# Performance work log

Hardware: AMD Instinct MI355X
Metric: run time of the kernel (lower is better)

## Reference

```python
import jax, jax.numpy as jnp
import numpy as np

H = 512      # hidden_size (hardcoded in prior split)
L = 3        # num_layers
NH = 8       # num_heads
B = 16384    # batch
LN_EPS = 1e-5


def layer_norm(x, g, b):
    m = x.mean(-1, keepdims=True)
    v = ((x - m) ** 2).mean(-1, keepdims=True)
    return (x - m) / jnp.sqrt(v + LN_EPS) * g + b


def cross_gen(src, tgt, ipw, ipb, qkv_w, qkv_b, ao_w, ao_b,
              ln1g, ln1b, ln2g, ln2b, f1w, f1b, f2w, f2b, opw, opb, rw):
    """CrossModalGenerator.forward(src, tgt) for the whole batch (seq_len == 1)."""
    bsz = src.shape[0]
    dh = H // NH
    x = src @ ipw.T + ipb  # input_proj
    for l in range(L):
        wq, wk, wv = jnp.split(qkv_w[l], 3, axis=0)
        bq, bk, bv = jnp.split(qkv_b[l], 3)
        q = (x @ wq.T + bq).reshape(bsz, NH, dh)
        k = (tgt @ wk.T + bk).reshape(bsz, NH, dh)
        v = (tgt @ wv.T + bv).reshape(bsz, NH, dh)
        # single key/value token -> softmax over 1 element == 1 (kept for faithful grads)
        scores = (q * k).sum(-1, keepdims=True) / jnp.sqrt(jnp.float32(dh))  # [B,NH,1]
        w = jax.nn.softmax(scores, axis=-1)
        attn = (w * v).reshape(bsz, H)
        attn = attn @ ao_w[l].T + ao_b[l]  # MHA out_proj
        x = layer_norm(x + attn, ln1g[l], ln1b[l])
        h = jax.nn.gelu(x @ f1w[l].T + f1b[l], approximate=False)
        h = h @ f2w[l].T + f2b[l]
        x = layer_norm(x + h, ln2g[l], ln2b[l])
    gen = x @ opw.T + opb  # output_proj
    return rw * tgt + (1.0 - rw) * gen


def setup_inputs() -> dict:
    key = jax.random.key(0)
    ks = iter(jax.random.split(key, 40))
    nk = lambda: next(ks)
    s = jnp.float32(0.02)  # weight scale for numerical sanity
    f32 = jnp.float32
    return {
        "image_features": jax.random.normal(nk(), (B, H), f32),
        "text_features": jax.random.normal(nk(), (B, H), f32),
        "g_ipw": jax.random.normal(nk(), (2, H, H), f32) * s,
        "g_ipb": jnp.zeros((2, H), f32),
        "g_qkv_w": jax.random.normal(nk(), (2, L, 3 * H, H), f32) * s,
        "g_qkv_b": jnp.zeros((2, L, 3 * H), f32),
        "g_ao_w": jax.random.normal(nk(), (2, L, H, H), f32) * s,
        "g_ao_b": jnp.zeros((2, L, H), f32),
        "g_ln1g": jnp.ones((2, L, H), f32),
        "g_ln1b": jnp.zeros((2, L, H), f32),
        "g_ln2g": jnp.ones((2, L, H), f32),
        "g_ln2b": jnp.zeros((2, L, H), f32),
        "g_f1w": jax.random.normal(nk(), (2, L, 4 * H, H), f32) * s,
        "g_f1b": jnp.zeros((2, L, 4 * H), f32),
        "g_f2w": jax.random.normal(nk(), (2, L, H, 4 * H), f32) * s,
        "g_f2b": jnp.zeros((2, L, H), f32),
        "g_opw": jax.random.normal(nk(), (2, H, H), f32) * s,
        "g_opb": jnp.zeros((2, H), f32),
        "g_rw": jnp.full((2,), 0.5, f32),  # residual_weight per generator
        "prior_w1": jax.random.normal(nk(), (2 * H, H), f32) * s,
        "prior_b1": jnp.zeros((2 * H,), f32),
        "prior_w2": jax.random.normal(nk(), (2 * H, 2 * H), f32) * s,
        "prior_b2": jnp.zeros((2 * H,), f32),
        "prior_emb": jax.random.normal(nk(), (1, H), f32),
        "missing_type": jax.random.randint(nk(), (B,), 0, 4, jnp.int32),
    }


def reference(image_features, text_features, g_ipw, g_ipb, g_qkv_w, g_qkv_b,
              g_ao_w, g_ao_b, g_ln1g, g_ln1b, g_ln2g, g_ln2b, g_f1w, g_f1b,
              g_f2w, g_f2b, g_opw, g_opb, g_rw, prior_w1, prior_b1, prior_w2,
              prior_b2, prior_emb, missing_type):
    def gen(i, src, tgt):
        return cross_gen(src, tgt, g_ipw[i], g_ipb[i], g_qkv_w[i], g_qkv_b[i],
                         g_ao_w[i], g_ao_b[i], g_ln1g[i], g_ln1b[i],
                         g_ln2g[i], g_ln2b[i], g_f1w[i], g_f1b[i],
                         g_f2w[i], g_f2b[i], g_opw[i], g_opb[i], g_rw[i])

    # MoE-style dense dispatch: run both generators on the full batch, select by type.
    gen_text = gen(0, image_features, text_features)  # img_to_text, missing_type==1
    gen_img = gen(1, text_features, image_features)   # text_to_img, missing_type==2

    prior = jax.nn.gelu(prior_emb @ prior_w1.T + prior_b1, approximate=False)
    prior = prior @ prior_w2.T + prior_b2  # [1, 2H]
    p_img, p_text = prior[:, :H], prior[:, H:]

    mt = missing_type[:, None]
    enhanced_img = jnp.where(mt == 2, gen_img, image_features)
    enhanced_img = jnp.where(mt == 3, p_img, enhanced_img)
    enhanced_text = jnp.where(mt == 1, gen_text, text_features)
    enhanced_text = jnp.where(mt == 3, p_text, enhanced_text)
    return enhanced_img, enhanced_text
```

## Files before the change

### kernel.cpp

```cpp
#include <hip/hip_runtime.h>
#include <hip/hip_bf16.h>
#include <math.h>

#define BDIM 16384
#define HDIM 512

typedef __bf16 bf16;
typedef float f32x4 __attribute__((ext_vector_type(4)));
typedef __bf16 bf16x8 __attribute__((ext_vector_type(8)));
typedef __bf16 bf16x4 __attribute__((ext_vector_type(4)));


__device__ __forceinline__ void gload16(const bf16* g, bf16* l) {
  __builtin_amdgcn_global_load_lds((const __attribute__((address_space(1))) void*)g,
                                   (__attribute__((address_space(3))) void*)l, 16, 0, 0);
}

__device__ __forceinline__ float gelu_exact(float x) {
  return 0.5f * x * (1.0f + erff(x * 0.70710678118654752f));
}
__device__ __forceinline__ float gelu_fast(float x) {
  float u = x * (0.7978845608f + 0.0356774081f * x * x);
  float e = __expf(2.f * u);
  float t = 1.f - 2.f / (e + 1.f);
  return 0.5f * x * (1.f + t);
}


__global__ void cvt_f32_bf16(const float* __restrict__ src, bf16* __restrict__ dst, int n4) {
  int i = blockIdx.x * blockDim.x + threadIdx.x;
  if (i >= n4) return;
  f32x4 v = *(const f32x4*)(src + (size_t)i * 4);
  bf16x4 o;
  o[0] = (bf16)v[0]; o[1] = (bf16)v[1]; o[2] = (bf16)v[2]; o[3] = (bf16)v[3];
  *(bf16x4*)(dst + (size_t)i * 4) = o;
}

__global__ void cvt_wvT(const float* __restrict__ qkv, bf16* __restrict__ dst) {
  __shared__ float t[32][33];
  int il = blockIdx.z;
  int bm = blockIdx.x * 32;
  int bk = blockIdx.y * 32;
  const float* s = qkv + (size_t)il * 786432 + 524288;
  int tx = threadIdx.x & 31, ty = threadIdx.x >> 5;
#pragma unroll
  for (int j = 0; j < 4; ++j)
    t[ty * 4 + j][tx] = s[(size_t)(bm + ty * 4 + j) * 512 + bk + tx];
  __syncthreads();
  bf16* d = dst + (size_t)il * 262144;
#pragma unroll
  for (int j = 0; j < 4; ++j)
    d[(size_t)(bk + ty * 4 + j) * 512 + bm + tx] = (bf16)t[tx][ty * 4 + j];
}

__global__ void zfill(float* __restrict__ p, int n) {
  int i = blockIdx.x * 256 + threadIdx.x;
  if (i < n) p[i] = 0.f;
}

__global__ void bias_combine(const float* __restrict__ aow, const float* __restrict__ qkvb,
                             const float* __restrict__ aob, float* __restrict__ bc) {
  int gid = blockIdx.x * 4 + (threadIdx.x >> 6);
  int il = gid >> 9;
  int lane = threadIdx.x & 63;
  const float* ar = aow + (size_t)gid * 512 + lane * 8;
  const float* bv = qkvb + il * 1536 + 1024 + lane * 8;
  float s = 0.f;
#pragma unroll
  for (int i = 0; i < 8; ++i) s += ar[i] * bv[i];
#pragma unroll
  for (int off = 32; off > 0; off >>= 1) s += __shfl_xor(s, off);
  if (lane == 0) bc[gid] = s + aob[gid];
}


template<int ACT, bool RES, int K>
__launch_bounds__(256, 2)
__global__ void gemm_q(const bf16* __restrict__ A, long long Az,
                       const bf16* __restrict__ W, long long Wz,
                       const float* __restrict__ bias, long long bz,
                       const bf16* X, long long Xz,
                       bf16* C, long long Cz, int ldc) {
  __shared__ bf16 lds[3][12288];
  const long long z = blockIdx.z;
  A += z * Az; W += z * Wz; bias += z * bz; C += z * Cz;
  if (RES) X += z * Xz;
  const int tid = threadIdx.x, lane = tid & 63, wid = tid >> 6;
  const int brow = blockIdx.x * 128, bcol = blockIdx.y * 256;
  const int wn = wid * 64, lr = lane & 15, kg = lane >> 4;
  const int ko = (kg ^ ((lr >> 1) & 3)) << 3;

  f32x4 acc[8][4] = {};

  const int sco = (((tid & 3) ^ ((tid >> 3) & 3)) << 3);
  const bf16* Ag = A + (size_t)(brow + (tid >> 2)) * K + sco;
  const bf16* Wg = W + (size_t)(bcol + (tid >> 2)) * K + sco;
  auto SA = [&](int s, int kt, int u) {
    gload16(Ag + (size_t)u * 64 * K + kt * 32, &lds[s][u * 2048 + wid * 512]);
  };
  auto SB = [&](int s, int kt, int u) {
    gload16(Wg + (size_t)u * 64 * K + kt * 32, &lds[s][4096 + u * 2048 + wid * 512]);
  };

  const int nt = K / 32;
  SA(0,0,0); SA(0,0,1); SB(0,0,0); SB(0,0,1); SB(0,0,2); SB(0,0,3);
  SA(1,1,0); SA(1,1,1); SB(1,1,0); SB(1,1,1); SB(1,1,2); SB(1,1,3);

  int slot = 0;
  for (int t = 0; t < nt; ++t) {
    int s2 = slot + 2; if (s2 >= 3) s2 -= 3;
    const bf16* LA = &lds[slot][0];
    const bf16* LB = &lds[slot][4096];
    if (t + 2 < nt) { SA(s2,t+2,0); SA(s2,t+2,1); SB(s2,t+2,0); SB(s2,t+2,1); }
    if (t + 2 < nt)      asm volatile("s_waitcnt vmcnt(10)" ::: "memory");
    else if (t + 1 < nt) asm volatile("s_waitcnt vmcnt(6)" ::: "memory");
    else                 asm volatile("s_waitcnt vmcnt(0)" ::: "memory");
    __builtin_amdgcn_s_barrier();
    bf16x8 a[8], b0, b1;
#pragma unroll
    for (int m = 0; m < 8; ++m) a[m] = *(const bf16x8*)(LA + ((m*16+lr)<<5) + ko);
    b0 = *(const bf16x8*)(LB + ((wn + lr)<<5) + ko);
    b1 = *(const bf16x8*)(LB + ((wn + 16 + lr)<<5) + ko);
    __builtin_amdgcn_s_setprio(1);
#pragma unroll
    for (int m = 0; m < 8; ++m) {
      acc[m][0] = __builtin_amdgcn_mfma_f32_16x16x32_bf16(b0, a[m], acc[m][0], 0, 0, 0);
      acc[m][1] = __builtin_amdgcn_mfma_f32_16x16x32_bf16(b1, a[m], acc[m][1], 0, 0, 0);
    }
    __builtin_amdgcn_s_setprio(0);
    asm volatile("" ::: "memory");
    __builtin_amdgcn_s_barrier();
    if (t + 2 < nt) { SB(s2,t+2,2); SB(s2,t+2,3); }
    bf16x8 b2 = *(const bf16x8*)(LB + ((wn + 32 + lr)<<5) + ko);
    bf16x8 b3 = *(const bf16x8*)(LB + ((wn + 48 + lr)<<5) + ko);
    __builtin_amdgcn_s_setprio(1);
#pragma unroll
    for (int m = 0; m < 8; ++m) {
      acc[m][2] = __builtin_amdgcn_mfma_f32_16x16x32_bf16(b2, a[m], acc[m][2], 0, 0, 0);
      acc[m][3] = __builtin_amdgcn_mfma_f32_16x16x32_bf16(b3, a[m], acc[m][3], 0, 0, 0);
    }
    __builtin_amdgcn_s_setprio(0);
    asm volatile("" ::: "memory");
    __builtin_amdgcn_s_barrier();
    slot += 1; if (slot >= 3) slot = 0;
  }

  f32x4 bv4[4];
#pragma unroll
  for (int n = 0; n < 4; ++n)
    bv4[n] = *(const f32x4*)(bias + bcol + wn + n * 16 + kg * 4);
#pragma unroll
  for (int m = 0; m < 8; ++m) {
    int row = brow + m * 16 + lr;
#pragma unroll
    for (int n = 0; n < 4; ++n) {
      int col = bcol + wn + n * 16 + kg * 4;
      f32x4 v;
#pragma unroll
      for (int j = 0; j < 4; ++j) {
        float t = acc[m][n][j] + bv4[n][j];
        if (ACT == 1) t = gelu_fast(t);
        v[j] = t;
      }
      if (RES) {
        bf16x4 xv = *(const bf16x4*)(X + (size_t)row * 512 + col);
#pragma unroll
        for (int j = 0; j < 4; ++j) v[j] += (float)xv[j];
      }
      bf16x4 o;
#pragma unroll
      for (int j = 0; j < 4; ++j) o[j] = (bf16)v[j];
      *(bf16x4*)(C + (size_t)row * ldc + col) = o;
    }
  }
}


__launch_bounds__(256)
__global__ void gemm128(const bf16* __restrict__ A, long long Az, int lda,
                        const bf16* __restrict__ W, long long Wz,
                        const float* __restrict__ bias, long long bz,
                        bf16* __restrict__ C, long long Cz, int ldc, int K) {
  __shared__ bf16 As[128 * 64];
  __shared__ bf16 Bs[128 * 64];
  const long long z = blockIdx.z;
  A += z * Az; W += z * Wz; bias += z * bz; C += z * Cz;
  const int tid = threadIdx.x;
  const int lane = tid & 63;
  const int wid = tid >> 6;
  const int brow = blockIdx.x * 128;
  const int bcol = blockIdx.y * 128;
  const int wr = (wid >> 1) * 64;
  const int wc = (wid & 1) * 64;
  const int lr = lane & 15;
  const int kg = lane >> 4;
  f32x4 acc[4][4] = {};
  const bf16* Abase = A + (size_t)(brow + (tid >> 3)) * lda + ((tid & 7) << 3);
  const bf16* Wbase = W + (size_t)(bcol + (tid >> 3)) * K + ((tid & 7) << 3);
  bf16* AsDst = As + wid * 512;
  bf16* BsDst = Bs + wid * 512;
  for (int k0 = 0; k0 < K; k0 += 64) {
#pragma unroll
    for (int j = 0; j < 4; ++j) {
      gload16(Abase + (size_t)j * 32 * lda + k0, AsDst + j * 2048);
      gload16(Wbase + (size_t)j * 32 * K + k0, BsDst + j * 2048);
    }
    __syncthreads();
#pragma unroll
    for (int kk = 0; kk < 64; kk += 32) {
      bf16x8 a[4], bq[4];
#pragma unroll
      for (int m = 0; m < 4; ++m)
        a[m] = *(const bf16x8*)(As + (wr + m * 16 + lr) * 64 + kk + kg * 8);
#pragma unroll
      for (int n = 0; n < 4; ++n)
        bq[n] = *(const bf16x8*)(Bs + (wc + n * 16 + lr) * 64 + kk + kg * 8);
#pragma unroll
      for (int m = 0; m < 4; ++m)
#pragma unroll
        for (int n = 0; n < 4; ++n)
          acc[m][n] = __builtin_amdgcn_mfma_f32_16x16x32_bf16(a[m], bq[n], acc[m][n], 0, 0, 0);
    }
    __syncthreads();
  }
  float bv[4];
#pragma unroll
  for (int n = 0; n < 4; ++n) bv[n] = bias[bcol + wc + n * 16 + lr];
#pragma unroll
  for (int m = 0; m < 4; ++m) {
    int row = brow + wr + m * 16 + kg * 4;
#pragma unroll
    for (int n = 0; n < 4; ++n) {
      int col = bcol + wc + n * 16 + lr;
#pragma unroll
      for (int j = 0; j < 4; ++j)
        C[(size_t)(row + j) * ldc + col] = (bf16)(acc[m][n][j] + bv[n]);
    }
  }
}


template<int MODE>
__global__ void ln_chain(const bf16* __restrict__ Y, const bf16* __restrict__ R,
                         const float* __restrict__ gA, const float* __restrict__ bA,
                         const float* __restrict__ gB, const float* __restrict__ bB,
                         bf16* __restrict__ O) {
  int lane = threadIdx.x & 63;
  int row = blockIdx.x * 4 + (threadIdx.x >> 6);
  int gen = row >> 14;
  size_t base = (size_t)row * HDIM + lane * 8;
  bf16x8 yv = *(const bf16x8*)(Y + base);
  float v[8], s = 0.f, q = 0.f;
#pragma unroll
  for (int i = 0; i < 8; ++i) { v[i] = (float)yv[i]; s += v[i]; q += v[i] * v[i]; }
#pragma unroll
  for (int off = 32; off > 0; off >>= 1) { s += __shfl_xor(s, off); q += __shfl_xor(q, off); }
  float mean = s * (1.f / HDIM);
  float rstd = rsqrtf(q * (1.f / HDIM) - mean * mean + 1e-5f);
  const float* gAp = gA + gen * 1536 + lane * 8;
  const float* bAp = bA + gen * 1536 + lane * 8;
  if (MODE == 0) {
    bf16x8 o;
#pragma unroll
    for (int i = 0; i < 8; ++i) o[i] = (bf16)((v[i] - mean) * rstd * gAp[i] + bAp[i]);
    *(bf16x8*)(O + base) = o;
    return;
  }
  bf16x8 rv = *(const bf16x8*)(R + base);
  float u[8]; s = 0.f; q = 0.f;
#pragma unroll
  for (int i = 0; i < 8; ++i) {
    u[i] = (v[i] - mean) * rstd * gAp[i] + bAp[i] + (float)rv[i];
    s += u[i]; q += u[i] * u[i];
  }
#pragma unroll
  for (int off = 32; off > 0; off >>= 1) { s += __shfl_xor(s, off); q += __shfl_xor(q, off); }
  float m2 = s * (1.f / HDIM);
  float r2 = rsqrtf(q * (1.f / HDIM) - m2 * m2 + 1e-5f);
  const float* gBp = gB + gen * 1536 + lane * 8;
  const float* bBp = bB + gen * 1536 + lane * 8;
  bf16x8 o;
#pragma unroll
  for (int i = 0; i < 8; ++i) o[i] = (bf16)((u[i] - m2) * r2 * gBp[i] + bBp[i]);
  *(bf16x8*)(O + base) = o;
}


__global__ void prior_fc1(const float* __restrict__ emb, const float* __restrict__ w1,
                          const float* __restrict__ b1, float* __restrict__ h) {
  int j = blockIdx.x * 4 + (threadIdx.x >> 6);
  int lane = threadIdx.x & 63;
  const float* wr = w1 + (size_t)j * 512 + lane * 8;
  const float* e = emb + lane * 8;
  float s = 0.f;
#pragma unroll
  for (int i = 0; i < 8; ++i) s += e[i] * wr[i];
#pragma unroll
  for (int off = 32; off > 0; off >>= 1) s += __shfl_xor(s, off);
  if (lane == 0) h[j] = gelu_exact(s + b1[j]);
}

__global__ void prior_fc2(const float* __restrict__ h, const float* __restrict__ w2,
                          const float* __restrict__ b2, float* __restrict__ p) {
  int j = blockIdx.x * 4 + (threadIdx.x >> 6);
  int lane = threadIdx.x & 63;
  const float* wr = w2 + (size_t)j * 1024 + lane * 16;
  const float* e = h + lane * 16;
  float s = 0.f;
#pragma unroll
  for (int i = 0; i < 16; ++i) s += e[i] * wr[i];
#pragma unroll
  for (int off = 32; off > 0; off >>= 1) s += __shfl_xor(s, off);
  if (lane == 0) p[j] = s + b2[j];
}


__global__ void combine(const float* __restrict__ img, const float* __restrict__ txt,
                        const bf16* __restrict__ gen_t, const bf16* __restrict__ gen_i,
                        const float* __restrict__ prior, const int* __restrict__ mt,
                        const float* __restrict__ rw, float* __restrict__ out) {
  int i4 = blockIdx.x * blockDim.x + threadIdx.x;
  if (i4 >= BDIM * 128) return;
  int bb = i4 >> 7;
  int c = (i4 & 127) << 2;
  size_t idx = (size_t)bb * HDIM + c;
  int m = mt[bb];
  f32x4 iv = *(const f32x4*)(img + idx);
  f32x4 tv = *(const f32x4*)(txt + idx);
  f32x4 oi = iv, ot = tv;
  if (m == 2) {
    float r = rw[1];
    bf16x4 gv = *(const bf16x4*)(gen_i + idx);
#pragma unroll
    for (int k = 0; k < 4; ++k) oi[k] = r * iv[k] + (1.f - r) * (float)gv[k];
  } else if (m == 3) {
    oi = *(const f32x4*)(prior + c);
  }
  if (m == 1) {
    float r = rw[0];
    bf16x4 gv = *(const bf16x4*)(gen_t + idx);
#pragma unroll
    for (int k = 0; k < 4; ++k) ot[k] = r * tv[k] + (1.f - r) * (float)gv[k];
  } else if (m == 3) {
    ot = *(const f32x4*)(prior + 512 + c);
  }
  *(f32x4*)(out + idx) = oi;
  *(f32x4*)(out + (size_t)BDIM * HDIM + idx) = ot;
}


extern "C" void kernel_launch(void* const* d_in, const int* in_sizes, int n_in,
                              void* d_out, int out_size, void* d_ws, size_t ws_size,
                              hipStream_t stream) {
  const float* img  = (const float*)d_in[0];
  const float* txt  = (const float*)d_in[1];
  const float* ipw  = (const float*)d_in[2];
  const float* ipb  = (const float*)d_in[3];
  const float* qkvw = (const float*)d_in[4];
  const float* qkvb = (const float*)d_in[5];
  const float* aow  = (const float*)d_in[6];
  const float* aob  = (const float*)d_in[7];
  const float* ln1g = (const float*)d_in[8];
  const float* ln1b = (const float*)d_in[9];
  const float* ln2g = (const float*)d_in[10];
  const float* ln2b = (const float*)d_in[11];
  const float* f1w  = (const float*)d_in[12];
  const float* f1b  = (const float*)d_in[13];
  const float* f2w  = (const float*)d_in[14];
  const float* f2b  = (const float*)d_in[15];
  const float* opw  = (const float*)d_in[16];
  const float* opb  = (const float*)d_in[17];
  const float* rw   = (const float*)d_in[18];
  const float* pw1  = (const float*)d_in[19];
  const float* pb1  = (const float*)d_in[20];
  const float* pw2  = (const float*)d_in[21];
  const float* pb2  = (const float*)d_in[22];
  const float* pemb = (const float*)d_in[23];
  const int*   mt   = (const int*)d_in[24];
  float* out = (float*)d_out;

  const size_t B = BDIM;
  char* ws = (char*)d_ws;
  size_t off = 0;
  auto alloc = [&](size_t bytes) -> char* {
    char* p = ws + off;
    off += (bytes + 255) & ~(size_t)255;
    return p;
  };
  bf16* src_bf = (bf16*)alloc(2 * B * 512 * 2);
  bf16* ipw_bf = (bf16*)alloc((size_t)2 * 262144 * 2);
  bf16* wvT_bf = (bf16*)alloc((size_t)6 * 262144 * 2);
  bf16* ao_bf  = (bf16*)alloc((size_t)6 * 262144 * 2);
  bf16* f1_bf  = (bf16*)alloc((size_t)6 * 1048576 * 2);
  bf16* f2_bf  = (bf16*)alloc((size_t)6 * 1048576 * 2);
  bf16* op_bf  = (bf16*)alloc((size_t)2 * 262144 * 2);
  bf16* Wc_bf  = (bf16*)alloc((size_t)6 * 262144 * 2);
  float* bc    = (float*)alloc(6 * 512 * 4);
  float* zeros = (float*)alloc(512 * 4);
  float* ph    = (float*)alloc(1024 * 4);
  float* pout  = (float*)alloc(1024 * 4);
  bf16* xn     = (bf16*)alloc(2 * B * 512 * 2);
  bf16* bufA   = (bf16*)alloc(2 * B * 512 * 2);
  bf16* bufB   = (bf16*)alloc(2 * B * 512 * 2);
  bf16* h      = (bf16*)d_out;

  auto cvt = [&](const float* s, bf16* d, size_t n) {
    int n4 = (int)(n / 4);
    cvt_f32_bf16<<<(n4 + 255) / 256, 256, 0, stream>>>(s, d, n4);
  };
  cvt(img, src_bf, B * 512);
  cvt(txt, src_bf + B * 512, B * 512);
  cvt(ipw, ipw_bf, 2 * 262144);
  cvt(aow, ao_bf, 6 * 262144);
  cvt(f1w, f1_bf, 6 * 1048576);
  cvt(f2w, f2_bf, 6 * 1048576);
  cvt(opw, op_bf, 2 * 262144);
  cvt_wvT<<<dim3(16, 16, 6), 256, 0, stream>>>(qkvw, wvT_bf);
  zfill<<<2, 256, 0, stream>>>(zeros, 512);
  bias_combine<<<768, 256, 0, stream>>>(aow, qkvb, aob, bc);
  gemm128<<<dim3(4, 4, 6), 256, 0, stream>>>(ao_bf, 262144, 512, wvT_bf, 262144,
                                             zeros, 0, Wc_bf, 262144, 512, 512);
  prior_fc1<<<256, 256, 0, stream>>>(pemb, pw1, pb1, ph);
  prior_fc2<<<256, 256, 0, stream>>>(ph, pw2, pb2, pout);

  const long long BS = (long long)B * 512;

  auto attn = [&](int l, bf16* dst) {
    gemm_q<0, false, 512><<<dim3(128, 2, 2), 256, 0, stream>>>(
        src_bf + BS, -BS, Wc_bf + (size_t)l * 262144, 786432,
        bc + l * 512, 1536, nullptr, 0, dst, BS, 512);
  };
  attn(0, bufA);
  attn(1, bufB);

  gemm_q<0, true, 512><<<dim3(128, 2, 2), 256, 0, stream>>>(
      src_bf, BS, ipw_bf, 262144, ipb, 512, bufA, BS, xn, BS, 512);
  ln_chain<0><<<2 * BDIM / 4, 256, 0, stream>>>(xn, nullptr, ln1g, ln1b,
                                                nullptr, nullptr, xn);
  attn(2, bufA);

  for (int l = 0; l < 3; ++l) {
    for (int i = 0; i < 2; ++i) {
      size_t il = (size_t)i * 3 + l;
      gemm_q<1, false, 512><<<dim3(128, 8, 1), 256, 0, stream>>>(
          xn + (size_t)i * BS, 0, f1_bf + il * 1048576, 0,
          f1b + il * 2048, 0, nullptr, 0, h, 0, 2048);
      gemm_q<0, true, 2048><<<dim3(128, 2, 1), 256, 0, stream>>>(
          h, 0, f2_bf + il * 1048576, 0,
          f2b + il * 512, 0, xn + (size_t)i * BS, 0, xn + (size_t)i * BS, 0, 512);
    }
    if (l < 2) {
      bf16* attnNext = (l == 0) ? bufB : bufA;
      ln_chain<1><<<2 * BDIM / 4, 256, 0, stream>>>(
          xn, attnNext, ln2g + l * 512, ln2b + l * 512,
          ln1g + (l + 1) * 512, ln1b + (l + 1) * 512, xn);
    } else {
      ln_chain<0><<<2 * BDIM / 4, 256, 0, stream>>>(
          xn, nullptr, ln2g + l * 512, ln2b + l * 512, nullptr, nullptr, xn);
    }
  }

  gemm_q<0, false, 512><<<dim3(128, 2, 2), 256, 0, stream>>>(
      xn, BS, op_bf, 262144, opb, 512, nullptr, 0, bufB, BS, 512);

  combine<<<(BDIM * 128 + 255) / 256, 256, 0, stream>>>(img, txt, bufB, bufB + BS,
                                                        pout, mt, rw, out);
}
```

Baseline: 931.7 us.

## Fuse FFN up/down GEMMs into one kernel keeping hidden activations in LDS

Replaces the separate FC1 (with GELU) and FC2 (with residual) GEMM launches per generator with a single gemm_mlp kernel. Each block owns 64 rows and walks the 2048 hidden dimension in 128-wide chunks, writing GELU output into LDS and immediately accumulating the FC2 product, so the 16384x2048 hidden tensor never goes to global memory. Both generators now share one launch through the z dimension. The GELU approximation is also rewritten as an exp2/rcp sigmoid form. The fused kernel uses about 124KB of LDS and a hand-tuned vmcnt wait schedule, which limits occupancy and is fragile to get right.

```diff
diff --git a/kernel.cpp b/kernel.cpp
--- a/kernel.cpp
+++ b/kernel.cpp
@@ -10,20 +10,25 @@
 typedef __bf16 bf16x8 __attribute__((ext_vector_type(8)));
 typedef __bf16 bf16x4 __attribute__((ext_vector_type(4)));
 
+#define WAITV(N) asm volatile("s_waitcnt vmcnt(" #N ")" ::: "memory")
+
 
 __device__ __forceinline__ void gload16(const bf16* g, bf16* l) {
   __builtin_amdgcn_global_load_lds((const __attribute__((address_space(1))) void*)g,
                                    (__attribute__((address_space(3))) void*)l, 16, 0, 0);
 }
+__device__ __forceinline__ void gload4(const bf16* g, bf16* l) {
+  __builtin_amdgcn_global_load_lds((const __attribute__((address_space(1))) void*)g,
+                                   (__attribute__((address_space(3))) void*)l, 4, 0, 0);
+}
 
 __device__ __forceinline__ float gelu_exact(float x) {
   return 0.5f * x * (1.0f + erff(x * 0.70710678118654752f));
 }
-__device__ __forceinline__ float gelu_fast(float x) {
-  float u = x * (0.7978845608f + 0.0356774081f * x * x);
-  float e = __expf(2.f * u);
-  float t = 1.f - 2.f / (e + 1.f);
-  return 0.5f * x * (1.f + t);
+__device__ __forceinline__ float gelu_fast2(float x) {
+  float x3 = x * x * x;
+  float e = exp2f(fmaf(-0.1029432f, x3, -2.3022082f * x));
+  return x * __builtin_amdgcn_rcpf(1.f + e);
 }
 
 
@@ -112,9 +117,9 @@
     const bf16* LA = &lds[slot][0];
     const bf16* LB = &lds[slot][4096];
     if (t + 2 < nt) { SA(s2,t+2,0); SA(s2,t+2,1); SB(s2,t+2,0); SB(s2,t+2,1); }
-    if (t + 2 < nt)      asm volatile("s_waitcnt vmcnt(10)" ::: "memory");
-    else if (t + 1 < nt) asm volatile("s_waitcnt vmcnt(6)" ::: "memory");
-    else                 asm volatile("s_waitcnt vmcnt(0)" ::: "memory");
+    if (t + 2 < nt)      WAITV(10);
+    else if (t + 1 < nt) WAITV(6);
+    else                 WAITV(0);
     __builtin_amdgcn_s_barrier();
     bf16x8 a[8], b0, b1;
 #pragma unroll
@@ -159,7 +164,7 @@
 #pragma unroll
       for (int j = 0; j < 4; ++j) {
         float t = acc[m][n][j] + bv4[n][j];
-        if (ACT == 1) t = gelu_fast(t);
+        if (ACT == 1) t = gelu_fast2(t);
         v[j] = t;
       }
       if (RES) {
@@ -173,6 +178,217 @@
       *(bf16x4*)(C + (size_t)row * ldc + col) = o;
     }
   }
+}
+
+
+__launch_bounds__(512, 2)
+__global__ void gemm_mlp(const bf16* __restrict__ Xg, long long Xz,
+                         const bf16* __restrict__ W1g, long long W1z,
+                         const float* __restrict__ b1g, long long b1z,
+                         const bf16* __restrict__ W2g, long long W2z,
+                         const float* __restrict__ b2g, long long b2z,
+                         bf16* O, long long Oz) {
+  __shared__ bf16 lds[63488];
+  const long long z = blockIdx.z;
+  const bf16* X = Xg + z * Xz;
+  W1g += z * W1z; b1g += z * b1z; W2g += z * W2z; b2g += z * b2z; O += z * Oz;
+
+  const int tid = threadIdx.x, lane = tid & 63, wid = tid >> 6;
+  const int brow = blockIdx.x * 64;
+  const int lr = lane & 15, kg = lane >> 4;
+  const int ko = (kg ^ ((lr >> 1) & 3)) << 3;
+
+  constexpr int AR  = 0;
+  constexpr int W1R = 6144;
+  constexpr int HB  = 18432;
+  constexpr int W2R = 26624;
+  float* B1 = (float*)(lds + 59392);
+
+  {
+    f32x4 bv = *(const f32x4*)(b1g + tid * 4);
+    *(f32x4*)(B1 + tid * 4) = bv;
+  }
+
+  const int sco16 = (((tid & 3) ^ ((tid >> 3) & 3)) << 3);
+  const int scoA  = ((((tid >> 2) & 3) ^ ((tid >> 5) & 3)) << 3) + ((tid & 3) << 1);
+  const bf16* Ag0 = X + (size_t)(brow + (tid >> 4)) * 512 + scoA;
+  const bf16* Ag1 = Ag0 + (size_t)32 * 512;
+  const bf16* W1c = W1g + (size_t)(tid >> 2) * 512 + sco16;
+  const bf16* W2c = W2g + (size_t)(tid >> 2) * 2048 + sco16;
+
+  auto SA = [&](int sl, int ks) {
+    gload4(Ag0 + ks * 32, lds + AR + sl * 2048 + wid * 128);
+    gload4(Ag1 + ks * 32, lds + AR + sl * 2048 + 1024 + wid * 128);
+  };
+  auto SW1 = [&](int sl, int ks, const bf16* w1p) {
+    gload16(w1p + ks * 32, lds + W1R + sl * 4096 + wid * 512);
+  };
+  auto SW2 = [&](int sl, int j, const bf16* w2p) {
+#pragma unroll
+    for (int u = 0; u < 4; ++u)
+      gload16(w2p + (size_t)u * 128 * 2048 + j * 32,
+              lds + W2R + sl * 16384 + u * 4096 + wid * 512);
+  };
+
+  f32x4 acc2[4][4] = {};
+
+  SA(0, 0); SW1(0, 0, W1c);
+  SA(1, 1); SW1(1, 1, W1c);
+  __syncthreads();
+
+  int sb = 0;
+  for (int c = 0; c < 16; ++c) {
+    const bf16* W1n = W1c + 65536;
+    f32x4 acc1[4] = {};
+
+#pragma unroll
+    for (int ks = 0; ks < 16; ++ks) {
+      int sl = ks % 3 + sb;       if (sl >= 3) sl -= 3;
+      int s2 = (ks + 2) % 3 + sb; if (s2 >= 3) s2 -= 3;
+      if (ks < 14) { SA(s2, ks + 2); SW1(s2, ks + 2, W1c); }
+      if (ks == 8)  SW2(0, 0, W2c);
+      if (ks == 10) SW2(1, 1, W2c);
+      if (ks < 8 || ks == 13)  WAITV(6);
+      else if (ks == 10)       WAITV(14);
+      else if (ks == 14)       WAITV(3);
+      else if (ks == 15)       WAITV(0);
+      else                     WAITV(10);
+      __builtin_amdgcn_s_barrier();
+      bf16x8 b1f = *(const bf16x8*)(lds + W1R + sl * 4096 + ((wid * 16 + lr) << 5) + ko);
+      bf16x8 a0 = *(const bf16x8*)(lds + AR + sl * 2048 + ((lr) << 5) + ko);
+      bf16x8 a1 = *(const bf16x8*)(lds + AR + sl * 2048 + ((16 + lr) << 5) + ko);
+      bf16x8 a2 = *(const bf16x8*)(lds + AR + sl * 2048 + ((32 + lr) << 5) + ko);
+      bf16x8 a3 = *(const bf16x8*)(lds + AR + sl * 2048 + ((48 + lr) << 5) + ko);
+      __builtin_amdgcn_s_setprio(1);
+      acc1[0] = __builtin_amdgcn_mfma_f32_16x16x32_bf16(b1f, a0, acc1[0], 0, 0, 0);
+      acc1[1] = __builtin_amdgcn_mfma_f32_16x16x32_bf16(b1f, a1, acc1[1], 0, 0, 0);
+      acc1[2] = __builtin_amdgcn_mfma_f32_16x16x32_bf16(b1f, a2, acc1[2], 0, 0, 0);
+      acc1[3] = __builtin_amdgcn_mfma_f32_16x16x32_bf16(b1f, a3, acc1[3], 0, 0, 0);
+      __builtin_amdgcn_s_setprio(0);
+      asm volatile("" ::: "memory");
+      __builtin_amdgcn_s_barrier();
+    }
+
+    {
+      f32x4 b1v = *(const f32x4*)(B1 + c * 128 + wid * 16 + kg * 4);
+      int colb = wid * 16 + kg * 4;
+      int hw = HB + ((colb >> 5) * 2048)
+             + ((((colb >> 3) & 3) ^ ((lr >> 1) & 3)) << 3) + (colb & 7);
+#pragma unroll
+      for (int m = 0; m < 4; ++m) {
+        bf16x4 hv;
+#pragma unroll
+        for (int j = 0; j < 4; ++j) hv[j] = (bf16)gelu_fast2(acc1[m][j] + b1v[j]);
+        *(bf16x4*)(lds + hw + ((m * 16 + lr) << 5)) = hv;
+      }
+    }
+    __syncthreads();
+
+    int sbn = sb + 1;  if (sbn >= 3) sbn -= 3;
+    int sb2 = sbn + 1; if (sb2 >= 3) sb2 -= 3;
+    const bool more = (c + 1 < 16);
+#pragma unroll
+    for (int j = 0; j < 4; ++j) {
+      if (j == 2) {
+        if (more) { SA(sb2, 1); SW1(sb2, 1, W1n); }
+        if (more) WAITV(10); else WAITV(4);
+        __builtin_amdgcn_s_barrier();
+      } else if (j == 3) {
+        if (more) WAITV(6); else WAITV(0);
+        __builtin_amdgcn_s_barrier();
+      }
+      bf16x8 bw0 = *(const bf16x8*)(lds + W2R + (j & 1) * 16384 + ((wid * 64 + lr) << 5) + ko);
+      bf16x8 bw1 = *(const bf16x8*)(lds + W2R + (j & 1) * 16384 + ((wid * 64 + 16 + lr) << 5) + ko);
+      bf16x8 bw2 = *(const bf16x8*)(lds + W2R + (j & 1) * 16384 + ((wid * 64 + 32 + lr) << 5) + ko);
+      bf16x8 bw3 = *(const bf16x8*)(lds + W2R + (j & 1) * 16384 + ((wid * 64 + 48 + lr) << 5) + ko);
+      bf16x8 ah[4];
+#pragma unroll
+      for (int m = 0; m < 4; ++m)
+        ah[m] = *(const bf16x8*)(lds + HB + j * 2048 + ((m * 16 + lr) << 5) + ko);
+      __builtin_amdgcn_s_setprio(1);
+#pragma unroll
+      for (int m = 0; m < 4; ++m) {
+        acc2[m][0] = __builtin_amdgcn_mfma_f32_16x16x32_bf16(bw0, ah[m], acc2[m][0], 0, 0, 0);
+        acc2[m][1] = __builtin_amdgcn_mfma_f32_16x16x32_bf16(bw1, ah[m], acc2[m][1], 0, 0, 0);
+        acc2[m][2] = __builtin_amdgcn_mfma_f32_16x16x32_bf16(bw2, ah[m], acc2[m][2], 0, 0, 0);
+        acc2[m][3] = __builtin_amdgcn_mfma_f32_16x16x32_bf16(bw3, ah[m], acc2[m][3], 0, 0, 0);
+      }
+      __builtin_amdgcn_s_setprio(0);
+      asm volatile("" ::: "memory");
+      __builtin_amdgcn_s_barrier();
+      if (j == 0) { SW2(0, 2, W2c); }
+      if (j == 1) { SW2(1, 3, W2c); if (more) { SA(sbn, 0); SW1(sbn, 0, W1n); } }
+    }
+
+    W1c = W1n;
+    W2c += 128;
+    sb = sbn;
+  }
+
+  f32x4 b2v[4];
+#pragma unroll
+  for (int n = 0; n < 4; ++n)
+    b2v[n] = *(const f32x4*)(b2g + wid * 64 + n * 16 + kg * 4);
+#pragma unroll
+  for (int m = 0; m < 4; ++m) {
+    int row = brow + m * 16 + lr;
+#pragma unroll
+    for (int n = 0; n < 4; ++n) {
+      int col = wid * 64 + n * 16 + kg * 4;
+      bf16x4 xv = *(const bf16x4*)(X + (size_t)row * 512 + col);
+      bf16x4 o;
+#pragma unroll
+      for (int j = 0; j < 4; ++j)
+        o[j] = (bf16)(acc2[m][n][j] + b2v[n][j] + (float)xv[j]);
+      *(bf16x4*)(O + (size_t)row * 512 + col) = o;
+    }
+  }
+}
+
+
+template<int MODE>
+__global__ void ln_chain(const bf16* __restrict__ Y, const bf16* __restrict__ R,
+                         const float* __restrict__ gA, const float* __restrict__ bA,
+                         const float* __restrict__ gB, const float* __restrict__ bB,
+                         bf16* __restrict__ O) {
+  int lane = threadIdx.x & 63;
+  int row = blockIdx.x * 4 + (threadIdx.x >> 6);
+  int gen = row >> 14;
+  size_t base = (size_t)row * HDIM + lane * 8;
+  bf16x8 yv = *(const bf16x8*)(Y + base);
+  float v[8], s = 0.f, q = 0.f;
+#pragma unroll
+  for (int i = 0; i < 8; ++i) { v[i] = (float)yv[i]; s += v[i]; q += v[i] * v[i]; }
+#pragma unroll
+  for (int off = 32; off > 0; off >>= 1) { s += __shfl_xor(s, off); q += __shfl_xor(q, off); }
+  float mean = s * (1.f / HDIM);
+  float rstd = rsqrtf(q * (1.f / HDIM) - mean * mean + 1e-5f);
+  const float* gAp = gA + gen * 1536 + lane * 8;
+  const float* bAp = bA + gen * 1536 + lane * 8;
+  if (MODE == 0) {
+    bf16x8 o;
+#pragma unroll
+    for (int i = 0; i < 8; ++i) o[i] = (bf16)((v[i] - mean) * rstd * gAp[i] + bAp[i]);
+    *(bf16x8*)(O + base) = o;
+    return;
+  }
+  bf16x8 rv = *(const bf16x8*)(R + base);
+  float u[8]; s = 0.f; q = 0.f;
+#pragma unroll
+  for (int i = 0; i < 8; ++i) {
+    u[i] = (v[i] - mean) * rstd * gAp[i] + bAp[i] + (float)rv[i];
+    s += u[i]; q += u[i] * u[i];
+  }
+#pragma unroll
+  for (int off = 32; off > 0; off >>= 1) { s += __shfl_xor(s, off); q += __shfl_xor(q, off); }
+  float m2 = s * (1.f / HDIM);
+  float r2 = rsqrtf(q * (1.f / HDIM) - m2 * m2 + 1e-5f);
+  const float* gBp = gB + gen * 1536 + lane * 8;
+  const float* bBp = bB + gen * 1536 + lane * 8;
+  bf16x8 o;
+#pragma unroll
+  for (int i = 0; i < 8; ++i) o[i] = (bf16)((u[i] - m2) * r2 * gBp[i] + bBp[i]);
+  *(bf16x8*)(O + base) = o;
 }
 
 
@@ -237,52 +453,6 @@
         C[(size_t)(row + j) * ldc + col] = (bf16)(acc[m][n][j] + bv[n]);
     }
   }
-}
-
-
-template<int MODE>
-__global__ void ln_chain(const bf16* __restrict__ Y, const bf16* __restrict__ R,
-                         const float* __restrict__ gA, const float* __restrict__ bA,
-                         const float* __restrict__ gB, const float* __restrict__ bB,
-                         bf16* __restrict__ O) {
-  int lane = threadIdx.x & 63;
-  int row = blockIdx.x * 4 + (threadIdx.x >> 6);
-  int gen = row >> 14;
-  size_t base = (size_t)row * HDIM + lane * 8;
-  bf16x8 yv = *(const bf16x8*)(Y + base);
-  float v[8], s = 0.f, q = 0.f;
-#pragma unroll
-  for (int i = 0; i < 8; ++i) { v[i] = (float)yv[i]; s += v[i]; q += v[i] * v[i]; }
-#pragma unroll
-  for (int off = 32; off > 0; off >>= 1) { s += __shfl_xor(s, off); q += __shfl_xor(q, off); }
-  float mean = s * (1.f / HDIM);
-  float rstd = rsqrtf(q * (1.f / HDIM) - mean * mean + 1e-5f);
-  const float* gAp = gA + gen * 1536 + lane * 8;
-  const float* bAp = bA + gen * 1536 + lane * 8;
-  if (MODE == 0) {
-    bf16x8 o;
-#pragma unroll
-    for (int i = 0; i < 8; ++i) o[i] = (bf16)((v[i] - mean) * rstd * gAp[i] + bAp[i]);
-    *(bf16x8*)(O + base) = o;
-    return;
-  }
-  bf16x8 rv = *(const bf16x8*)(R + base);
-  float u[8]; s = 0.f; q = 0.f;
-#pragma unroll
-  for (int i = 0; i < 8; ++i) {
-    u[i] = (v[i] - mean) * rstd * gAp[i] + bAp[i] + (float)rv[i];
-    s += u[i]; q += u[i] * u[i];
-  }
-#pragma unroll
-  for (int off = 32; off > 0; off >>= 1) { s += __shfl_xor(s, off); q += __shfl_xor(q, off); }
-  float m2 = s * (1.f / HDIM);
-  float r2 = rsqrtf(q * (1.f / HDIM) - m2 * m2 + 1e-5f);
-  const float* gBp = gB + gen * 1536 + lane * 8;
-  const float* bBp = bB + gen * 1536 + lane * 8;
-  bf16x8 o;
-#pragma unroll
-  for (int i = 0; i < 8; ++i) o[i] = (bf16)((u[i] - m2) * r2 * gBp[i] + bBp[i]);
-  *(bf16x8*)(O + base) = o;
 }
 
 
@@ -402,7 +572,6 @@
   bf16* xn     = (bf16*)alloc(2 * B * 512 * 2);
   bf16* bufA   = (bf16*)alloc(2 * B * 512 * 2);
   bf16* bufB   = (bf16*)alloc(2 * B * 512 * 2);
-  bf16* h      = (bf16*)d_out;
 
   auto cvt = [&](const float* s, bf16* d, size_t n) {
     int n4 = (int)(n / 4);
@@ -440,15 +609,13 @@
   attn(2, bufA);
 
   for (int l = 0; l < 3; ++l) {
-    for (int i = 0; i < 2; ++i) {
-      size_t il = (size_t)i * 3 + l;
-      gemm_q<1, false, 512><<<dim3(128, 8, 1), 256, 0, stream>>>(
-          xn + (size_t)i * BS, 0, f1_bf + il * 1048576, 0,
-          f1b + il * 2048, 0, nullptr, 0, h, 0, 2048);
-      gemm_q<0, true, 2048><<<dim3(128, 2, 1), 256, 0, stream>>>(
-          h, 0, f2_bf + il * 1048576, 0,
-          f2b + il * 512, 0, xn + (size_t)i * BS, 0, xn + (size_t)i * BS, 0, 512);
-    }
+    gemm_mlp<<<dim3(256, 1, 2), 512, 0, stream>>>(
+        xn, BS,
+        f1_bf + (size_t)l * 1048576, 3145728,
+        f1b + l * 2048, 6144,
+        f2_bf + (size_t)l * 1048576, 3145728,
+        f2b + l * 512, 1536,
+        xn, BS);
     if (l < 2) {
       bf16* attnNext = (l == 0) ? bufB : bufA;
       ln_chain<1><<<2 * BDIM / 4, 256, 0, stream>>>(
```

Result: slower. 1.117 ms (+19.9%).

## Batch both generators' FFN GEMMs per launch, simplify GEMM k-loop, cheaper GELU

Applied to the files above, without the earlier changes.

The two generators' FFN1/FFN2 GEMMs are now issued as single launches with a z-dimension of 2, using the output buffer and a new workspace region as the two hidden buffers. This halves the FFN launch count and doubles the grid size per launch. The attention GEMMs are recomputed just in time into a shared scratch buffer, which frees the two extra activation buffers. The GEMM k-loop now issues all six stage loads at once and runs a single MFMA phase per k-tile with one fewer barrier. GELU uses a sigmoid-form tanh approximation built on exp2 and rcp, which changes numerics slightly.

```diff
diff --git a/kernel.cpp b/kernel.cpp
--- a/kernel.cpp
+++ b/kernel.cpp
@@ -10,6 +10,8 @@
 typedef __bf16 bf16x8 __attribute__((ext_vector_type(8)));
 typedef __bf16 bf16x4 __attribute__((ext_vector_type(4)));
 
+#define WAITV(N) asm volatile("s_waitcnt vmcnt(" #N ")" ::: "memory")
+
 
 __device__ __forceinline__ void gload16(const bf16* g, bf16* l) {
   __builtin_amdgcn_global_load_lds((const __attribute__((address_space(1))) void*)g,
@@ -19,11 +21,10 @@
 __device__ __forceinline__ float gelu_exact(float x) {
   return 0.5f * x * (1.0f + erff(x * 0.70710678118654752f));
 }
-__device__ __forceinline__ float gelu_fast(float x) {
-  float u = x * (0.7978845608f + 0.0356774081f * x * x);
-  float e = __expf(2.f * u);
-  float t = 1.f - 2.f / (e + 1.f);
-  return 0.5f * x * (1.f + t);
+__device__ __forceinline__ float gelu_fast2(float x) {
+  float x3 = x * x * x;
+  float e = exp2f(fmaf(-0.1029432f, x3, -2.3022082f * x));
+  return x * __builtin_amdgcn_rcpf(1.f + e);
 }
 
 
@@ -95,50 +96,39 @@
   const int sco = (((tid & 3) ^ ((tid >> 3) & 3)) << 3);
   const bf16* Ag = A + (size_t)(brow + (tid >> 2)) * K + sco;
   const bf16* Wg = W + (size_t)(bcol + (tid >> 2)) * K + sco;
-  auto SA = [&](int s, int kt, int u) {
-    gload16(Ag + (size_t)u * 64 * K + kt * 32, &lds[s][u * 2048 + wid * 512]);
+  auto STAGE = [&](int s, int kt) {
+#pragma unroll
+    for (int u = 0; u < 2; ++u)
+      gload16(Ag + (size_t)u * 64 * K + kt * 32, &lds[s][u * 2048 + wid * 512]);
+#pragma unroll
+    for (int u = 0; u < 4; ++u)
+      gload16(Wg + (size_t)u * 64 * K + kt * 32, &lds[s][4096 + u * 2048 + wid * 512]);
   };
-  auto SB = [&](int s, int kt, int u) {
-    gload16(Wg + (size_t)u * 64 * K + kt * 32, &lds[s][4096 + u * 2048 + wid * 512]);
-  };
 
   const int nt = K / 32;
-  SA(0,0,0); SA(0,0,1); SB(0,0,0); SB(0,0,1); SB(0,0,2); SB(0,0,3);
-  SA(1,1,0); SA(1,1,1); SB(1,1,0); SB(1,1,1); SB(1,1,2); SB(1,1,3);
+  STAGE(0, 0);
+  STAGE(1, 1);
 
   int slot = 0;
   for (int t = 0; t < nt; ++t) {
     int s2 = slot + 2; if (s2 >= 3) s2 -= 3;
     const bf16* LA = &lds[slot][0];
     const bf16* LB = &lds[slot][4096];
-    if (t + 2 < nt) { SA(s2,t+2,0); SA(s2,t+2,1); SB(s2,t+2,0); SB(s2,t+2,1); }
-    if (t + 2 < nt)      asm volatile("s_waitcnt vmcnt(10)" ::: "memory");
-    else if (t + 1 < nt) asm volatile("s_waitcnt vmcnt(6)" ::: "memory");
-    else                 asm volatile("s_waitcnt vmcnt(0)" ::: "memory");
+    if (t + 2 < nt) { STAGE(s2, t + 2); WAITV(12); }
+    else if (t + 1 < nt) WAITV(6);
+    else WAITV(0);
     __builtin_amdgcn_s_barrier();
-    bf16x8 a[8], b0, b1;
-#pragma unroll
-    for (int m = 0; m < 8; ++m) a[m] = *(const bf16x8*)(LA + ((m*16+lr)<<5) + ko);
-    b0 = *(const bf16x8*)(LB + ((wn + lr)<<5) + ko);
-    b1 = *(const bf16x8*)(LB + ((wn + 16 + lr)<<5) + ko);
+    bf16x8 a[8], b[4];
+#pragma unroll
+    for (int m = 0; m < 8; ++m) a[m] = *(const bf16x8*)(LA + ((m * 16 + lr) << 5) + ko);
+#pragma unroll
+    for (int n = 0; n < 4; ++n) b[n] = *(const bf16x8*)(LB + ((wn + n * 16 + lr) << 5) + ko);
     __builtin_amdgcn_s_setprio(1);
 #pragma unroll
-    for (int m = 0; m < 8; ++m) {
-      acc[m][0] = __builtin_amdgcn_mfma_f32_16x16x32_bf16(b0, a[m], acc[m][0], 0, 0, 0);
-      acc[m][1] = __builtin_amdgcn_mfma_f32_16x16x32_bf16(b1, a[m], acc[m][1], 0, 0, 0);
-    }
-    __builtin_amdgcn_s_setprio(0);
-    asm volatile("" ::: "memory");
-    __builtin_amdgcn_s_barrier();
-    if (t + 2 < nt) { SB(s2,t+2,2); SB(s2,t+2,3); }
-    bf16x8 b2 = *(const bf16x8*)(LB + ((wn + 32 + lr)<<5) + ko);
-    bf16x8 b3 = *(const bf16x8*)(LB + ((wn + 48 + lr)<<5) + ko);
-    __builtin_amdgcn_s_setprio(1);
-#pragma unroll
-    for (int m = 0; m < 8; ++m) {
-      acc[m][2] = __builtin_amdgcn_mfma_f32_16x16x32_bf16(b2, a[m], acc[m][2], 0, 0, 0);
-      acc[m][3] = __builtin_amdgcn_mfma_f32_16x16x32_bf16(b3, a[m], acc[m][3], 0, 0, 0);
-    }
+    for (int m = 0; m < 8; ++m)
+#pragma unroll
+      for (int n = 0; n < 4; ++n)
+        acc[m][n] = __builtin_amdgcn_mfma_f32_16x16x32_bf16(b[n], a[m], acc[m][n], 0, 0, 0);
     __builtin_amdgcn_s_setprio(0);
     asm volatile("" ::: "memory");
     __builtin_amdgcn_s_barrier();
@@ -159,7 +149,7 @@
 #pragma unroll
       for (int j = 0; j < 4; ++j) {
         float t = acc[m][n][j] + bv4[n][j];
-        if (ACT == 1) t = gelu_fast(t);
+        if (ACT == 1) t = gelu_fast2(t);
         v[j] = t;
       }
       if (RES) {
@@ -173,6 +163,52 @@
       *(bf16x4*)(C + (size_t)row * ldc + col) = o;
     }
   }
+}
+
+
+template<int MODE>
+__global__ void ln_chain(const bf16* __restrict__ Y, const bf16* __restrict__ R,
+                         const float* __restrict__ gA, const float* __restrict__ bA,
+                         const float* __restrict__ gB, const float* __restrict__ bB,
+                         bf16* __restrict__ O) {
+  int lane = threadIdx.x & 63;
+  int row = blockIdx.x * 4 + (threadIdx.x >> 6);
+  int gen = row >> 14;
+  size_t base = (size_t)row * HDIM + lane * 8;
+  bf16x8 yv = *(const bf16x8*)(Y + base);
+  float v[8], s = 0.f, q = 0.f;
+#pragma unroll
+  for (int i = 0; i < 8; ++i) { v[i] = (float)yv[i]; s += v[i]; q += v[i] * v[i]; }
+#pragma unroll
+  for (int off = 32; off > 0; off >>= 1) { s += __shfl_xor(s, off); q += __shfl_xor(q, off); }
+  float mean = s * (1.f / HDIM);
+  float rstd = rsqrtf(q * (1.f / HDIM) - mean * mean + 1e-5f);
+  const float* gAp = gA + gen * 1536 + lane * 8;
+  const float* bAp = bA + gen * 1536 + lane * 8;
+  if (MODE == 0) {
+    bf16x8 o;
+#pragma unroll
+    for (int i = 0; i < 8; ++i) o[i] = (bf16)((v[i] - mean) * rstd * gAp[i] + bAp[i]);
+    *(bf16x8*)(O + base) = o;
+    return;
+  }
+  bf16x8 rv = *(const bf16x8*)(R + base);
+  float u[8]; s = 0.f; q = 0.f;
+#pragma unroll
+  for (int i = 0; i < 8; ++i) {
+    u[i] = (v[i] - mean) * rstd * gAp[i] + bAp[i] + (float)rv[i];
+    s += u[i]; q += u[i] * u[i];
+  }
+#pragma unroll
+  for (int off = 32; off > 0; off >>= 1) { s += __shfl_xor(s, off); q += __shfl_xor(q, off); }
+  float m2 = s * (1.f / HDIM);
+  float r2 = rsqrtf(q * (1.f / HDIM) - m2 * m2 + 1e-5f);
+  const float* gBp = gB + gen * 1536 + lane * 8;
+  const float* bBp = bB + gen * 1536 + lane * 8;
+  bf16x8 o;
+#pragma unroll
+  for (int i = 0; i < 8; ++i) o[i] = (bf16)((u[i] - m2) * r2 * gBp[i] + bBp[i]);
+  *(bf16x8*)(O + base) = o;
 }
 
 
@@ -237,52 +273,6 @@
         C[(size_t)(row + j) * ldc + col] = (bf16)(acc[m][n][j] + bv[n]);
     }
   }
-}
-
-
-template<int MODE>
-__global__ void ln_chain(const bf16* __restrict__ Y, const bf16* __restrict__ R,
-                         const float* __restrict__ gA, const float* __restrict__ bA,
-                         const float* __restrict__ gB, const float* __restrict__ bB,
-                         bf16* __restrict__ O) {
-  int lane = threadIdx.x & 63;
-  int row = blockIdx.x * 4 + (threadIdx.x >> 6);
-  int gen = row >> 14;
-  size_t base = (size_t)row * HDIM + lane * 8;
-  bf16x8 yv = *(const bf16x8*)(Y + base);
-  float v[8], s = 0.f, q = 0.f;
-#pragma unroll
-  for (int i = 0; i < 8; ++i) { v[i] = (float)yv[i]; s += v[i]; q += v[i] * v[i]; }
-#pragma unroll
-  for (int off = 32; off > 0; off >>= 1) { s += __shfl_xor(s, off); q += __shfl_xor(q, off); }
-  float mean = s * (1.f / HDIM);
-  float rstd = rsqrtf(q * (1.f / HDIM) - mean * mean + 1e-5f);
-  const float* gAp = gA + gen * 1536 + lane * 8;
-  const float* bAp = bA + gen * 1536 + lane * 8;
-  if (MODE == 0) {
-    bf16x8 o;
-#pragma unroll
-    for (int i = 0; i < 8; ++i) o[i] = (bf16)((v[i] - mean) * rstd * gAp[i] + bAp[i]);
-    *(bf16x8*)(O + base) = o;
-    return;
-  }
-  bf16x8 rv = *(const bf16x8*)(R + base);
-  float u[8]; s = 0.f; q = 0.f;
-#pragma unroll
-  for (int i = 0; i < 8; ++i) {
-    u[i] = (v[i] - mean) * rstd * gAp[i] + bAp[i] + (float)rv[i];
-    s += u[i]; q += u[i] * u[i];
-  }
-#pragma unroll
-  for (int off = 32; off > 0; off >>= 1) { s += __shfl_xor(s, off); q += __shfl_xor(q, off); }
-  float m2 = s * (1.f / HDIM);
-  float r2 = rsqrtf(q * (1.f / HDIM) - m2 * m2 + 1e-5f);
-  const float* gBp = gB + gen * 1536 + lane * 8;
-  const float* bBp = bB + gen * 1536 + lane * 8;
-  bf16x8 o;
-#pragma unroll
-  for (int i = 0; i < 8; ++i) o[i] = (bf16)((u[i] - m2) * r2 * gBp[i] + bBp[i]);
-  *(bf16x8*)(O + base) = o;
 }
 
 
@@ -400,9 +390,9 @@
   float* ph    = (float*)alloc(1024 * 4);
   float* pout  = (float*)alloc(1024 * 4);
   bf16* xn     = (bf16*)alloc(2 * B * 512 * 2);
-  bf16* bufA   = (bf16*)alloc(2 * B * 512 * 2);
-  bf16* bufB   = (bf16*)alloc(2 * B * 512 * 2);
-  bf16* h      = (bf16*)d_out;
+  bf16* hreg   = (bf16*)alloc((size_t)B * 2048 * 2);
+  bf16* h0     = (bf16*)d_out;
+  const long long HZ = (long long)(hreg - h0);
 
   auto cvt = [&](const float* s, bf16* d, size_t n) {
     int n4 = (int)(n / 4);
@@ -425,34 +415,29 @@
 
   const long long BS = (long long)B * 512;
 
-  auto attn = [&](int l, bf16* dst) {
+  auto attn = [&](int l) {
     gemm_q<0, false, 512><<<dim3(128, 2, 2), 256, 0, stream>>>(
         src_bf + BS, -BS, Wc_bf + (size_t)l * 262144, 786432,
-        bc + l * 512, 1536, nullptr, 0, dst, BS, 512);
+        bc + l * 512, 1536, nullptr, 0, hreg, BS, 512);
   };
-  attn(0, bufA);
-  attn(1, bufB);
-
+
+  attn(0);
   gemm_q<0, true, 512><<<dim3(128, 2, 2), 256, 0, stream>>>(
-      src_bf, BS, ipw_bf, 262144, ipb, 512, bufA, BS, xn, BS, 512);
+      src_bf, BS, ipw_bf, 262144, ipb, 512, hreg, BS, xn, BS, 512);
   ln_chain<0><<<2 * BDIM / 4, 256, 0, stream>>>(xn, nullptr, ln1g, ln1b,
                                                 nullptr, nullptr, xn);
-  attn(2, bufA);
 
   for (int l = 0; l < 3; ++l) {
-    for (int i = 0; i < 2; ++i) {
-      size_t il = (size_t)i * 3 + l;
-      gemm_q<1, false, 512><<<dim3(128, 8, 1), 256, 0, stream>>>(
-          xn + (size_t)i * BS, 0, f1_bf + il * 1048576, 0,
-          f1b + il * 2048, 0, nullptr, 0, h, 0, 2048);
-      gemm_q<0, true, 2048><<<dim3(128, 2, 1), 256, 0, stream>>>(
-          h, 0, f2_bf + il * 1048576, 0,
-          f2b + il * 512, 0, xn + (size_t)i * BS, 0, xn + (size_t)i * BS, 0, 512);
-    }
+    gemm_q<1, false, 512><<<dim3(128, 8, 2), 256, 0, stream>>>(
+        xn, BS, f1_bf + (size_t)l * 1048576, 3145728,
+        f1b + l * 2048, 6144, nullptr, 0, h0, HZ, 2048);
+    gemm_q<0, true, 2048><<<dim3(128, 2, 2), 256, 0, stream>>>(
+        h0, HZ, f2_bf + (size_t)l * 1048576, 3145728,
+        f2b + l * 512, 1536, xn, BS, xn, BS, 512);
     if (l < 2) {
-      bf16* attnNext = (l == 0) ? bufB : bufA;
+      attn(l + 1);
       ln_chain<1><<<2 * BDIM / 4, 256, 0, stream>>>(
-          xn, attnNext, ln2g + l * 512, ln2b + l * 512,
+          xn, hreg, ln2g + l * 512, ln2b + l * 512,
           ln1g + (l + 1) * 512, ln1b + (l + 1) * 512, xn);
     } else {
       ln_chain<0><<<2 * BDIM / 4, 256, 0, stream>>>(
@@ -461,8 +446,8 @@
   }
 
   gemm_q<0, false, 512><<<dim3(128, 2, 2), 256, 0, stream>>>(
-      xn, BS, op_bf, 262144, opb, 512, nullptr, 0, bufB, BS, 512);
-
-  combine<<<(BDIM * 128 + 255) / 256, 256, 0, stream>>>(img, txt, bufB, bufB + BS,
+      xn, BS, op_bf, 262144, opb, 512, nullptr, 0, hreg, BS, 512);
+
+  combine<<<(BDIM * 128 + 255) / 256, 256, 0, stream>>>(img, txt, hreg, hreg + BS,
                                                         pout, mt, rw, out);
 }
```

Result: faster. 869.0 us, median of 2 (-6.7%).
